# Kernel optimization log

Hardware: AMD Instinct MI355X
Metric: run time of the kernel (lower is better)

Reference implementation:

```python
import jax, jax.numpy as jnp
import numpy as np

B, S, D, H = 4, 2048, 1024, 16
HD = D // H  # head_dim = 64


def setup_inputs() -> dict:
    key = jax.random.key(0)
    ks = jax.random.split(key, 6)
    scale = 0.02
    x = jax.random.normal(ks[0], (B, S, D), dtype=jnp.float32)
    # per-head projection weights, torch Linear is y = x @ W.T; store as [H, D, HD]
    Wq = jax.random.normal(ks[1], (H, D, HD), dtype=jnp.float32) * scale
    Wk = jax.random.normal(ks[2], (H, D, HD), dtype=jnp.float32) * scale
    Wv = jax.random.normal(ks[3], (H, D, HD), dtype=jnp.float32) * scale
    Wo = jax.random.normal(ks[4], (D, D), dtype=jnp.float32) * scale  # torch [out, in]
    bo = jax.random.normal(ks[5], (D,), dtype=jnp.float32) * scale
    return {"x": x, "Wq": Wq, "Wk": Wk, "Wv": Wv, "Wo": Wo, "bo": bo}


def reference(x, Wq, Wk, Wv, Wo, bo):
    # project: [B,S,D] x [H,D,HD] -> [B,H,S,HD]
    q = jnp.einsum("bsd,hde->bhse", x, Wq)
    k = jnp.einsum("bsd,hde->bhse", x, Wk)
    v = jnp.einsum("bsd,hde->bhse", x, Wv)
    scores = jnp.einsum("bhse,bhte->bhst", q, k) / jnp.sqrt(jnp.float32(HD))
    causal = jnp.tril(jnp.ones((S, S), dtype=bool))  # same as registered tril mask
    scores = jnp.where(causal, scores, -jnp.inf)
    w = jax.nn.softmax(scores, axis=-1)
    out = jnp.einsum("bhst,bhte->bhse", w, v)  # [B,H,S,HD]
    # concat heads along feature dim: [B,S,H*HD] = [B,S,D]
    out = out.transpose(0, 2, 1, 3).reshape(B, S, D)
    # output projection: torch Linear y = x @ W.T + b
    return jnp.einsum("bsd,od->bso", out, Wo) + bo
```

## Files before the change

### kernel.cpp

```cpp
#include <hip/hip_runtime.h>
#include <hip/hip_bf16.h>

typedef __bf16 bf16x8 __attribute__((ext_vector_type(8)));
typedef float f32x4 __attribute__((ext_vector_type(4)));
typedef unsigned short u16x4 __attribute__((ext_vector_type(4)));
typedef unsigned short u16x8 __attribute__((ext_vector_type(8)));
typedef unsigned uint4v __attribute__((ext_vector_type(4)));

#define B_ 4
#define S_ 2048
#define D_ 1024
#define H_ 16
#define HD_ 64

__device__ __forceinline__ unsigned short f2bf(float f) {
  unsigned u = __float_as_uint(f);
  u += 0x7fff + ((u >> 16) & 1);
  return (unsigned short)(u >> 16);
}

__device__ __forceinline__ void gload16(const void* g, void* l) {
  __builtin_amdgcn_global_load_lds((const __attribute__((address_space(1))) unsigned int*)g,
                                   (__attribute__((address_space(3))) unsigned int*)l,
                                   16, 0, 0);
}

__global__ void pack_x_k(const float* __restrict__ in, unsigned short* __restrict__ out, int n4) {
  int i = blockIdx.x * blockDim.x + threadIdx.x;
  int stride = gridDim.x * blockDim.x;
  for (; i < n4; i += stride) {
    float4 v = reinterpret_cast<const float4*>(in)[i];
    u16x4 o = {f2bf(v.x), f2bf(v.y), f2bf(v.z), f2bf(v.w)};
    reinterpret_cast<u16x4*>(out)[i] = o;
  }
}

__global__ void pack_wqkv_k(const float* __restrict__ Wq, const float* __restrict__ Wk,
                            const float* __restrict__ Wv, unsigned short* __restrict__ Wt) {
  int o = blockIdx.x * blockDim.x + threadIdx.x;
  int n = o >> 10;
  int d = o & 1023;
  const float* W = (n < 1024) ? Wq : (n < 2048) ? Wk : Wv;
  int nn = n & 1023;
  int h = nn >> 6, e = nn & 63;
  Wt[o] = f2bf(W[(h << 16) + (d << 6) + e]);
}

__global__ __launch_bounds__(512, 2) void gemm256_k(const unsigned short* __restrict__ A,
                                                    const unsigned short* __restrict__ Bt,
                                                    unsigned short* __restrict__ QK,
                                                    unsigned short* __restrict__ VT,
                                                    int M, int N, int K) {
  __shared__ __align__(16) unsigned short lA0[2][128 * 64];
  __shared__ __align__(16) unsigned short lA1[2][128 * 64];
  __shared__ __align__(16) unsigned short lB[2][192 * 64];
  const int tid = threadIdx.x;
  const int wid = tid >> 6, lane = tid & 63;
  const int r = lane & 15, g = lane >> 4;
  const int wm = wid >> 2, wn = wid & 3;

  const int i_hw = blockIdx.y * gridDim.x + blockIdx.x;
  const int xcd = i_hw & 7, j = i_hw >> 3;
  const long arow0 = (long)((xcd & 3) * 8 + (j & 7)) * 256;
  const long bcol0 = (long)((xcd >> 2) * 8 + (j >> 3)) * 192;

  const f32x4 z4 = {0.f, 0.f, 0.f, 0.f};
  f32x4 acc[8][3];
#pragma unroll
  for (int m = 0; m < 8; ++m)
#pragma unroll
    for (int n = 0; n < 3; ++n) acc[m][n] = z4;

  auto stage_half = [&](int kt, int which) {
    const unsigned short* src = (which == 2) ? Bt + bcol0 * K : A + (arow0 + 128 * which) * K;
    const int k0 = kt << 6;
    unsigned short* base = (which == 0) ? &lA0[kt & 1][0]
                         : (which == 1) ? &lA1[kt & 1][0] : &lB[kt & 1][0];
    const int nch = (which == 2) ? 3 : 2;
    for (int c = 0; c < nch; ++c) {
      const int jj = c * 512 + tid;
      const int row = jj >> 3, cc = jj & 7;
      const int ccs = cc ^ (row & 7);
      gload16(src + (long)row * K + k0 + ccs * 8, base + jj * 8);
    }
  };

  bf16x8 af[4][2], bv[3][2];
  auto read_a = [&](const unsigned short* lbase) {
#pragma unroll
    for (int i2 = 0; i2 < 4; ++i2)
#pragma unroll
      for (int kk = 0; kk < 2; ++kk) {
        const int rowh = (2 * i2 + wm) * 16 + r;
        af[i2][kk] = *(const bf16x8*)&lbase[rowh * 64 + (((kk << 2) + g) ^ (rowh & 7)) * 8];
      }
  };
  auto read_b = [&](int buf) {
#pragma unroll
    for (int j2 = 0; j2 < 3; ++j2)
#pragma unroll
      for (int kk = 0; kk < 2; ++kk) {
        const int rowh = (4 * j2 + wn) * 16 + r;
        bv[j2][kk] = *(const bf16x8*)&lB[buf][rowh * 64 + (((kk << 2) + g) ^ (rowh & 7)) * 8];
      }
  };
  auto mma_h = [&](int mh) {
    __builtin_amdgcn_s_setprio(1);
#pragma unroll
    for (int kk = 0; kk < 2; ++kk)
#pragma unroll
      for (int i2 = 0; i2 < 4; ++i2)
#pragma unroll
        for (int j2 = 0; j2 < 3; ++j2)
          acc[4 * mh + i2][j2] = __builtin_amdgcn_mfma_f32_16x16x32_bf16(
              af[i2][kk], bv[j2][kk], acc[4 * mh + i2][j2], 0, 0, 0);
    __builtin_amdgcn_s_setprio(0);
  };

  const int nk = K >> 6;
  stage_half(0, 0);
  stage_half(0, 2);
  stage_half(0, 1);
  asm volatile("s_waitcnt vmcnt(2)" ::: "memory");
  asm volatile("s_barrier" ::: "memory");

  for (int t = 0; t < nk; ++t) {
    const int buf = t & 1;
    const bool pre = (t + 1 < nk);
    read_a(&lA0[buf][0]);
    read_b(buf);
    if (pre) { stage_half(t + 1, 0); stage_half(t + 1, 2); }
    asm volatile("s_barrier" ::: "memory");
    mma_h(0);
    if (pre) asm volatile("s_waitcnt vmcnt(5)" ::: "memory");
    else     asm volatile("s_waitcnt vmcnt(0)" ::: "memory");
    asm volatile("s_waitcnt lgkmcnt(0)\n\ts_barrier" ::: "memory");
    read_a(&lA1[buf][0]);
    if (pre) stage_half(t + 1, 1);
    asm volatile("s_barrier" ::: "memory");
    mma_h(1);
    if (pre) asm volatile("s_waitcnt vmcnt(2)" ::: "memory");
    asm volatile("s_waitcnt lgkmcnt(0)\n\ts_barrier" ::: "memory");
  }

#pragma unroll
  for (int j2 = 0; j2 < 3; ++j2) {
    const long colb = bcol0 + (4 * j2 + wn) * 16;
    if (colb < 2048) {
#pragma unroll
      for (int m = 0; m < 8; ++m)
#pragma unroll
        for (int rr = 0; rr < 4; ++rr) {
          const long row = arow0 + (2 * m + wm) * 16 + g * 4 + rr;
          QK[row * 2048 + colb + r] = f2bf(acc[m][j2][rr]);
        }
    } else {
      const long vcol = colb - 2048 + r;
      const long h = vcol >> 6, e = vcol & 63;
#pragma unroll
      for (int m = 0; m < 8; ++m) {
        const long row0 = arow0 + (2 * m + wm) * 16 + g * 4;
        const long b = row0 >> 11, s = row0 & 2047;
        u16x4 w4;
#pragma unroll
        for (int rr = 0; rr < 4; ++rr) w4[rr] = f2bf(acc[m][j2][rr]);
        *(u16x4*)&VT[(((b << 4) + h) * 64 + e) * 2048 + s] = w4;
      }
    }
  }
}

__global__ __launch_bounds__(512, 2) void gemm_op_k(const unsigned short* __restrict__ A,
                                                    const unsigned short* __restrict__ Bt,
                                                    float* __restrict__ C,
                                                    const float* __restrict__ bias,
                                                    int M, int N, int K) {
  __shared__ __align__(16) unsigned short lA0[2][128 * 64];
  __shared__ __align__(16) unsigned short lA1[2][128 * 64];
  __shared__ __align__(16) unsigned short lB[2][128 * 64];
  const int tid = threadIdx.x;
  const int wid = tid >> 6, lane = tid & 63;
  const int r = lane & 15, g = lane >> 4;
  const int wm = wid >> 2, wn = wid & 3;

  const int i_hw = blockIdx.y * gridDim.x + blockIdx.x;
  const int xcd = i_hw & 7, j = i_hw >> 3;
  const long arow0 = (long)((xcd & 3) * 8 + (j & 7)) * 256;
  const long bcol0 = (long)((xcd >> 2) * 4 + (j >> 3)) * 128;

  const f32x4 z4 = {0.f, 0.f, 0.f, 0.f};
  f32x4 acc[8][2];
#pragma unroll
  for (int m = 0; m < 8; ++m)
#pragma unroll
    for (int n = 0; n < 2; ++n) acc[m][n] = z4;

  auto stage_half = [&](int kt, int which) {
    const unsigned short* src = (which == 2) ? Bt + bcol0 * K : A + (arow0 + 128 * which) * K;
    const int k0 = kt << 6;
    unsigned short* base = (which == 0) ? &lA0[kt & 1][0]
                         : (which == 1) ? &lA1[kt & 1][0] : &lB[kt & 1][0];
#pragma unroll
    for (int c = 0; c < 2; ++c) {
      const int jj = c * 512 + tid;
      const int row = jj >> 3, cc = jj & 7;
      const int ccs = cc ^ (row & 7);
      gload16(src + (long)row * K + k0 + ccs * 8, base + jj * 8);
    }
  };

  bf16x8 af[4][2], bv[2][2];
  auto read_a = [&](const unsigned short* lbase) {
#pragma unroll
    for (int i2 = 0; i2 < 4; ++i2)
#pragma unroll
      for (int kk = 0; kk < 2; ++kk) {
        const int rowh = (2 * i2 + wm) * 16 + r;
        af[i2][kk] = *(const bf16x8*)&lbase[rowh * 64 + (((kk << 2) + g) ^ (rowh & 7)) * 8];
      }
  };
  auto read_b = [&](int buf) {
#pragma unroll
    for (int j2 = 0; j2 < 2; ++j2)
#pragma unroll
      for (int kk = 0; kk < 2; ++kk) {
        const int rowh = (4 * j2 + wn) * 16 + r;
        bv[j2][kk] = *(const bf16x8*)&lB[buf][rowh * 64 + (((kk << 2) + g) ^ (rowh & 7)) * 8];
      }
  };
  auto mma_h = [&](int mh) {
    __builtin_amdgcn_s_setprio(1);
#pragma unroll
    for (int kk = 0; kk < 2; ++kk)
#pragma unroll
      for (int i2 = 0; i2 < 4; ++i2)
#pragma unroll
        for (int j2 = 0; j2 < 2; ++j2)
          acc[4 * mh + i2][j2] = __builtin_amdgcn_mfma_f32_16x16x32_bf16(
              af[i2][kk], bv[j2][kk], acc[4 * mh + i2][j2], 0, 0, 0);
    __builtin_amdgcn_s_setprio(0);
  };

  const int nk = K >> 6;
  stage_half(0, 0);
  stage_half(0, 2);
  stage_half(0, 1);
  asm volatile("s_waitcnt vmcnt(2)" ::: "memory");
  asm volatile("s_barrier" ::: "memory");

  for (int t = 0; t < nk; ++t) {
    const int buf = t & 1;
    const bool pre = (t + 1 < nk);
    read_a(&lA0[buf][0]);
    read_b(buf);
    if (pre) { stage_half(t + 1, 0); stage_half(t + 1, 2); }
    asm volatile("s_barrier" ::: "memory");
    mma_h(0);
    if (pre) asm volatile("s_waitcnt vmcnt(4)" ::: "memory");
    else     asm volatile("s_waitcnt vmcnt(0)" ::: "memory");
    asm volatile("s_waitcnt lgkmcnt(0)\n\ts_barrier" ::: "memory");
    read_a(&lA1[buf][0]);
    if (pre) stage_half(t + 1, 1);
    asm volatile("s_barrier" ::: "memory");
    mma_h(1);
    if (pre) asm volatile("s_waitcnt vmcnt(2)" ::: "memory");
    asm volatile("s_waitcnt lgkmcnt(0)\n\ts_barrier" ::: "memory");
  }

#pragma unroll
  for (int m = 0; m < 8; ++m)
#pragma unroll
    for (int n = 0; n < 2; ++n)
#pragma unroll
      for (int rr = 0; rr < 4; ++rr) {
        const long row = arow0 + (2 * m + wm) * 16 + g * 4 + rr;
        const long col = bcol0 + (4 * n + wn) * 16 + r;
        C[row * N + col] = acc[m][n][rr] + bias[col];
      }
}

__global__ __launch_bounds__(256, 2) void attn_k(const unsigned short* __restrict__ qk,
                                                 const unsigned short* __restrict__ vt,
                                                 unsigned short* __restrict__ out) {
  __shared__ __align__(16) unsigned short lK[2][64 * 64];
  __shared__ __align__(16) unsigned short lVt[2][64 * 64];

  const int tid = threadIdx.x, wid = tid >> 6, lane = tid & 63;
  const int r = lane & 15, g = lane >> 4;
  const int bh = blockIdx.x;
  const int b = bh >> 4, h = bh & 15;
  const int qb = 15 - (int)blockIdx.y;
  const int q0 = qb * 128;

  const unsigned short* Qg = qk + ((long)b * S_) * 2048 + h * 64;
  const unsigned short* Kg = Qg + 1024;
  const unsigned short* Vg = vt + ((long)(b * 16 + h)) * 64 * 2048;

  int qrow[2];
  bf16x8 qf[2][2];
#pragma unroll
  for (int qs = 0; qs < 2; ++qs) {
    qrow[qs] = q0 + qs * 64 + wid * 16 + r;
#pragma unroll
    for (int kk = 0; kk < 2; ++kk)
      qf[qs][kk] = *(const bf16x8*)&Qg[(long)qrow[qs] * 2048 + kk * 32 + g * 8];
  }

  const f32x4 z4 = {0.f, 0.f, 0.f, 0.f};
  f32x4 o[2][4];
#pragma unroll
  for (int qs = 0; qs < 2; ++qs)
#pragma unroll
    for (int nt = 0; nt < 4; ++nt) o[qs][nt] = z4;
  float m_i[2] = {-1e30f, -1e30f};
  float l_i[2] = {0.f, 0.f};

  const int srow = tid >> 3, scc = tid & 7;
  const int sccs = (scc ^ (srow & 7)) << 3;
  const unsigned short* kp = Kg + (long)srow * 2048 + sccs;
  const unsigned short* kp2 = Kg + (long)(srow + 32) * 2048 + sccs;
  const unsigned short* vp = Vg + (long)srow * 2048 + sccs;
  const unsigned short* vp2 = Vg + (long)(srow + 32) * 2048 + sccs;
  auto stage = [&](int buf, long koff, long voff) {
    gload16(kp + koff, &lK[buf][tid * 8]);
    gload16(kp2 + koff, &lK[buf][(256 + tid) * 8]);
    gload16(vp + voff, &lVt[buf][tid * 8]);
    gload16(vp2 + voff, &lVt[buf][(256 + tid) * 8]);
  };

  const int ntiles = (q0 >> 6) + 2;
  stage(0, 0, 0);

  for (int t = 0; t < ntiles; ++t) {
    const int cur = t & 1;
    __syncthreads();
    if (t + 1 < ntiles) stage(cur ^ 1, (long)(t + 1) * 64 * 2048, (long)(t + 1) * 64);

    const int t0 = t << 6;
    const bool act0 = (t < ntiles - 1);
    const bool diag0 = (t == ntiles - 2);
    const bool diag1 = (t == ntiles - 1);

    f32x4 st[2][4];
#pragma unroll
    for (int tt = 0; tt < 4; ++tt) { st[0][tt] = z4; st[1][tt] = z4; }
    __builtin_amdgcn_s_setprio(1);
#pragma unroll
    for (int kk = 0; kk < 2; ++kk)
#pragma unroll
      for (int tt = 0; tt < 4; ++tt) {
        const int row = tt * 16 + r, cc = kk * 4 + g;
        bf16x8 kf = *(const bf16x8*)&lK[cur][(row * 8 + (cc ^ (row & 7))) * 8];
        st[1][tt] = __builtin_amdgcn_mfma_f32_16x16x32_bf16(kf, qf[1][kk], st[1][tt], 0, 0, 0);
        if (act0)
          st[0][tt] = __builtin_amdgcn_mfma_f32_16x16x32_bf16(kf, qf[0][kk], st[0][tt], 0, 0, 0);
      }
    __builtin_amdgcn_s_setprio(0);

    bf16x8 pf[2][2];
    unsigned corr_bits[2] = {0x3f800000u, 0x3f800000u};
    bool dodef[2] = {true, true};
#pragma unroll
    for (int qs = 0; qs < 2; ++qs) {
      if (qs == 0 && !act0) continue;
      const bool diag = qs ? diag1 : diag0;
      float sv[16];
      if (diag) {
#pragma unroll
        for (int tt = 0; tt < 4; ++tt)
#pragma unroll
          for (int rg = 0; rg < 4; ++rg) {
            float s = st[qs][tt][rg];
            if (t0 + tt * 16 + g * 4 + rg > qrow[qs]) s = -1e30f;
            sv[tt * 4 + rg] = s;
          }
      } else {
#pragma unroll
        for (int tt = 0; tt < 4; ++tt)
#pragma unroll
          for (int rg = 0; rg < 4; ++rg) sv[tt * 4 + rg] = st[qs][tt][rg];
      }
      float h0 = fmaxf(fmaxf(fmaxf(sv[0], sv[1]), fmaxf(sv[2], sv[3])),
                       fmaxf(fmaxf(sv[4], sv[5]), fmaxf(sv[6], sv[7])));
      float h1 = fmaxf(fmaxf(fmaxf(sv[8], sv[9]), fmaxf(sv[10], sv[11])),
                       fmaxf(fmaxf(sv[12], sv[13]), fmaxf(sv[14], sv[15])));
      const float pmax = fmaxf(h0, h1);
      const bool defer = __all(pmax - m_i[qs] <= 64.f);
      float corr = 1.f;
      if (!defer) {
        float mx = fmaxf(pmax, m_i[qs]);
        mx = fmaxf(mx, __shfl_xor(mx, 16, 64));
        mx = fmaxf(mx, __shfl_xor(mx, 32, 64));
        corr = __expf((m_i[qs] - mx) * 0.125f);
        m_i[qs] = mx;
      }
      dodef[qs] = defer;
      corr_bits[qs] = __float_as_uint(corr);
      const float m8 = m_i[qs] * 0.125f;
      float p[16];
      float rs = 0.f;
#pragma unroll
      for (int i = 0; i < 16; ++i) {
        p[i] = __expf(__builtin_fmaf(sv[i], 0.125f, -m8));
        rs += p[i];
      }
      rs += __shfl_xor(rs, 16, 64);
      rs += __shfl_xor(rs, 32, 64);
      l_i[qs] = l_i[qs] * corr + rs;
      unsigned cw[4][2];
#pragma unroll
      for (int tt = 0; tt < 4; ++tt)
#pragma unroll
        for (int e = 0; e < 2; ++e)
          asm("v_cvt_pk_bf16_f32 %0, %1, %2"
              : "=v"(cw[tt][e]) : "v"(p[tt * 4 + 2 * e]), "v"(p[tt * 4 + 2 * e + 1]));
#pragma unroll
      for (int kk = 0; kk < 2; ++kk) {
        unsigned x0 = cw[2 * kk][0], y0 = cw[2 * kk + 1][0];
        unsigned x1 = cw[2 * kk][1], y1 = cw[2 * kk + 1][1];
        asm volatile("v_permlane32_swap_b32 %0, %1" : "+v"(x0), "+v"(y0));
        asm volatile("v_permlane16_swap_b32 %0, %1" : "+v"(x0), "+v"(y0));
        asm volatile("v_permlane32_swap_b32 %0, %1" : "+v"(x1), "+v"(y1));
        asm volatile("v_permlane16_swap_b32 %0, %1" : "+v"(x1), "+v"(y1));
        uint4v w = {x0, x1, y0, y1};
        pf[qs][kk] = *(bf16x8*)&w;
      }
    }
#pragma unroll
    for (int qs = 0; qs < 2; ++qs) {
      if (qs == 0 && !act0) continue;
      if (!dodef[qs]) {
        const float corr = __uint_as_float(corr_bits[qs]);
#pragma unroll
        for (int rr = 0; rr < 4; ++rr) {
          const float c = __shfl(corr, g * 4 + rr, 64);
#pragma unroll
          for (int nt = 0; nt < 4; ++nt) o[qs][nt][rr] *= c;
        }
      }
    }

    __builtin_amdgcn_s_setprio(1);
#pragma unroll
    for (int kk = 0; kk < 2; ++kk)
#pragma unroll
      for (int nt = 0; nt < 4; ++nt) {
        const int row = nt * 16 + r, cc = kk * 4 + g;
        const bf16x8 vf = *(const bf16x8*)&lVt[cur][(row * 8 + (cc ^ (row & 7))) * 8];
        o[1][nt] = __builtin_amdgcn_mfma_f32_16x16x32_bf16(pf[1][kk], vf, o[1][nt], 0, 0, 0);
        if (act0)
          o[0][nt] = __builtin_amdgcn_mfma_f32_16x16x32_bf16(pf[0][kk], vf, o[0][nt], 0, 0, 0);
      }
    __builtin_amdgcn_s_setprio(0);
  }

#pragma unroll
  for (int qs = 0; qs < 2; ++qs) {
    float linv[4];
#pragma unroll
    for (int rr = 0; rr < 4; ++rr)
      linv[rr] = 1.f / __shfl(l_i[qs], g * 4 + rr, 64);
#pragma unroll
    for (int nt = 0; nt < 4; ++nt)
#pragma unroll
      for (int rr = 0; rr < 4; ++rr) {
        const long s = q0 + qs * 64 + wid * 16 + g * 4 + rr;
        out[((long)b * S_ + s) * 1024 + h * 64 + nt * 16 + r] = f2bf(o[qs][nt][rr] * linv[rr]);
      }
  }
}

extern "C" void kernel_launch(void* const* d_in, const int* in_sizes, int n_in,
                              void* d_out, int out_size, void* d_ws, size_t ws_size,
                              hipStream_t stream) {
  const float* x = (const float*)d_in[0];
  const float* Wq = (const float*)d_in[1];
  const float* Wk = (const float*)d_in[2];
  const float* Wv = (const float*)d_in[3];
  const float* Wo = (const float*)d_in[4];
  const float* bo = (const float*)d_in[5];
  float* out = (float*)d_out;

  char* ws = (char*)d_ws;
  unsigned short* Xb = (unsigned short*)(ws);
  unsigned short* Wt = (unsigned short*)(ws + (16ul << 20));
  unsigned short* Wob = (unsigned short*)(ws + (22ul << 20));
  unsigned short* QK = (unsigned short*)(ws + (24ul << 20));
  unsigned short* VT = (unsigned short*)(ws + (56ul << 20));
  unsigned short* AO = (unsigned short*)(ws + (72ul << 20));

  pack_x_k<<<2048, 256, 0, stream>>>(x, Xb, (B_ * S_ * D_) / 4);
  pack_x_k<<<512, 256, 0, stream>>>(Wo, Wob, (D_ * D_) / 4);
  pack_wqkv_k<<<(3 * D_ * D_) / 256, 256, 0, stream>>>(Wq, Wk, Wv, Wt);

  gemm256_k<<<dim3(32, 16), 512, 0, stream>>>(Xb, Wt, QK, VT, B_ * S_, 3 * D_, D_);
  attn_k<<<dim3(64, 16), 256, 0, stream>>>(QK, VT, AO);
  gemm_op_k<<<dim3(32, 8), 512, 0, stream>>>(AO, Wob, out, bo, B_ * S_, D_, D_);
}
```

Before: 178.0 us.

## Shrink attention query tile from 128 to 64 rows per block

```diff
diff --git a/kernel.cpp b/kernel.cpp
--- a/kernel.cpp
+++ b/kernel.cpp
@@ -289,31 +289,25 @@
   const int r = lane & 15, g = lane >> 4;
   const int bh = blockIdx.x;
   const int b = bh >> 4, h = bh & 15;
-  const int qb = 15 - (int)blockIdx.y;
-  const int q0 = qb * 128;
+  const int qb = 31 - (int)blockIdx.y;
+  const int q0 = qb * 64;
 
   const unsigned short* Qg = qk + ((long)b * S_) * 2048 + h * 64;
   const unsigned short* Kg = Qg + 1024;
   const unsigned short* Vg = vt + ((long)(b * 16 + h)) * 64 * 2048;
 
-  int qrow[2];
-  bf16x8 qf[2][2];
-#pragma unroll
-  for (int qs = 0; qs < 2; ++qs) {
-    qrow[qs] = q0 + qs * 64 + wid * 16 + r;
-#pragma unroll
-    for (int kk = 0; kk < 2; ++kk)
-      qf[qs][kk] = *(const bf16x8*)&Qg[(long)qrow[qs] * 2048 + kk * 32 + g * 8];
-  }
+  const int qrow = q0 + wid * 16 + r;
+  bf16x8 qf[2];
+#pragma unroll
+  for (int kk = 0; kk < 2; ++kk)
+    qf[kk] = *(const bf16x8*)&Qg[(long)qrow * 2048 + kk * 32 + g * 8];
 
   const f32x4 z4 = {0.f, 0.f, 0.f, 0.f};
-  f32x4 o[2][4];
-#pragma unroll
-  for (int qs = 0; qs < 2; ++qs)
-#pragma unroll
-    for (int nt = 0; nt < 4; ++nt) o[qs][nt] = z4;
-  float m_i[2] = {-1e30f, -1e30f};
-  float l_i[2] = {0.f, 0.f};
+  f32x4 o[4];
+#pragma unroll
+  for (int nt = 0; nt < 4; ++nt) o[nt] = z4;
+  float m_i = -1e30f;
+  float l_i = 0.f;
 
   const int srow = tid >> 3, scc = tid & 7;
   const int sccs = (scc ^ (srow & 7)) << 3;
@@ -328,7 +322,7 @@
     gload16(vp2 + voff, &lVt[buf][(256 + tid) * 8]);
   };
 
-  const int ntiles = (q0 >> 6) + 2;
+  const int ntiles = qb + 1;
   stage(0, 0, 0);
 
   for (int t = 0; t < ntiles; ++t) {
@@ -337,13 +331,11 @@
     if (t + 1 < ntiles) stage(cur ^ 1, (long)(t + 1) * 64 * 2048, (long)(t + 1) * 64);
 
     const int t0 = t << 6;
-    const bool act0 = (t < ntiles - 1);
-    const bool diag0 = (t == ntiles - 2);
-    const bool diag1 = (t == ntiles - 1);
-
-    f32x4 st[2][4];
-#pragma unroll
-    for (int tt = 0; tt < 4; ++tt) { st[0][tt] = z4; st[1][tt] = z4; }
+    const bool diag = (t == ntiles - 1);
+
+    f32x4 st[4];
+#pragma unroll
+    for (int tt = 0; tt < 4; ++tt) st[tt] = z4;
     __builtin_amdgcn_s_setprio(1);
 #pragma unroll
     for (int kk = 0; kk < 2; ++kk)
@@ -351,92 +343,76 @@
       for (int tt = 0; tt < 4; ++tt) {
         const int row = tt * 16 + r, cc = kk * 4 + g;
         bf16x8 kf = *(const bf16x8*)&lK[cur][(row * 8 + (cc ^ (row & 7))) * 8];
-        st[1][tt] = __builtin_amdgcn_mfma_f32_16x16x32_bf16(kf, qf[1][kk], st[1][tt], 0, 0, 0);
-        if (act0)
-          st[0][tt] = __builtin_amdgcn_mfma_f32_16x16x32_bf16(kf, qf[0][kk], st[0][tt], 0, 0, 0);
+        st[tt] = __builtin_amdgcn_mfma_f32_16x16x32_bf16(kf, qf[kk], st[tt], 0, 0, 0);
       }
     __builtin_amdgcn_s_setprio(0);
 
-    bf16x8 pf[2][2];
-    unsigned corr_bits[2] = {0x3f800000u, 0x3f800000u};
-    bool dodef[2] = {true, true};
-#pragma unroll
-    for (int qs = 0; qs < 2; ++qs) {
-      if (qs == 0 && !act0) continue;
-      const bool diag = qs ? diag1 : diag0;
-      float sv[16];
-      if (diag) {
-#pragma unroll
-        for (int tt = 0; tt < 4; ++tt)
-#pragma unroll
-          for (int rg = 0; rg < 4; ++rg) {
-            float s = st[qs][tt][rg];
-            if (t0 + tt * 16 + g * 4 + rg > qrow[qs]) s = -1e30f;
-            sv[tt * 4 + rg] = s;
-          }
-      } else {
-#pragma unroll
-        for (int tt = 0; tt < 4; ++tt)
-#pragma unroll
-          for (int rg = 0; rg < 4; ++rg) sv[tt * 4 + rg] = st[qs][tt][rg];
-      }
-      float h0 = fmaxf(fmaxf(fmaxf(sv[0], sv[1]), fmaxf(sv[2], sv[3])),
-                       fmaxf(fmaxf(sv[4], sv[5]), fmaxf(sv[6], sv[7])));
-      float h1 = fmaxf(fmaxf(fmaxf(sv[8], sv[9]), fmaxf(sv[10], sv[11])),
-                       fmaxf(fmaxf(sv[12], sv[13]), fmaxf(sv[14], sv[15])));
-      const float pmax = fmaxf(h0, h1);
-      const bool defer = __all(pmax - m_i[qs] <= 64.f);
-      float corr = 1.f;
-      if (!defer) {
-        float mx = fmaxf(pmax, m_i[qs]);
-        mx = fmaxf(mx, __shfl_xor(mx, 16, 64));
-        mx = fmaxf(mx, __shfl_xor(mx, 32, 64));
-        corr = __expf((m_i[qs] - mx) * 0.125f);
-        m_i[qs] = mx;
-      }
-      dodef[qs] = defer;
-      corr_bits[qs] = __float_as_uint(corr);
-      const float m8 = m_i[qs] * 0.125f;
-      float p[16];
-      float rs = 0.f;
-#pragma unroll
-      for (int i = 0; i < 16; ++i) {
-        p[i] = __expf(__builtin_fmaf(sv[i], 0.125f, -m8));
-        rs += p[i];
-      }
-      rs += __shfl_xor(rs, 16, 64);
-      rs += __shfl_xor(rs, 32, 64);
-      l_i[qs] = l_i[qs] * corr + rs;
-      unsigned cw[4][2];
+    float sv[16];
+    if (diag) {
 #pragma unroll
       for (int tt = 0; tt < 4; ++tt)
 #pragma unroll
-        for (int e = 0; e < 2; ++e)
-          asm("v_cvt_pk_bf16_f32 %0, %1, %2"
-              : "=v"(cw[tt][e]) : "v"(p[tt * 4 + 2 * e]), "v"(p[tt * 4 + 2 * e + 1]));
-#pragma unroll
-      for (int kk = 0; kk < 2; ++kk) {
-        unsigned x0 = cw[2 * kk][0], y0 = cw[2 * kk + 1][0];
-        unsigned x1 = cw[2 * kk][1], y1 = cw[2 * kk + 1][1];
-        asm volatile("v_permlane32_swap_b32 %0, %1" : "+v"(x0), "+v"(y0));
-        asm volatile("v_permlane16_swap_b32 %0, %1" : "+v"(x0), "+v"(y0));
-        asm volatile("v_permlane32_swap_b32 %0, %1" : "+v"(x1), "+v"(y1));
-        asm volatile("v_permlane16_swap_b32 %0, %1" : "+v"(x1), "+v"(y1));
-        uint4v w = {x0, x1, y0, y1};
-        pf[qs][kk] = *(bf16x8*)&w;
-      }
-    }
-#pragma unroll
-    for (int qs = 0; qs < 2; ++qs) {
-      if (qs == 0 && !act0) continue;
-      if (!dodef[qs]) {
-        const float corr = __uint_as_float(corr_bits[qs]);
-#pragma unroll
-        for (int rr = 0; rr < 4; ++rr) {
-          const float c = __shfl(corr, g * 4 + rr, 64);
-#pragma unroll
-          for (int nt = 0; nt < 4; ++nt) o[qs][nt][rr] *= c;
+        for (int rg = 0; rg < 4; ++rg) {
+          float s = st[tt][rg];
+          if (t0 + tt * 16 + g * 4 + rg > qrow) s = -1e30f;
+          sv[tt * 4 + rg] = s;
         }
+    } else {
+#pragma unroll
+      for (int tt = 0; tt < 4; ++tt)
+#pragma unroll
+        for (int rg = 0; rg < 4; ++rg) sv[tt * 4 + rg] = st[tt][rg];
+    }
+    float h0 = fmaxf(fmaxf(fmaxf(sv[0], sv[1]), fmaxf(sv[2], sv[3])),
+                     fmaxf(fmaxf(sv[4], sv[5]), fmaxf(sv[6], sv[7])));
+    float h1 = fmaxf(fmaxf(fmaxf(sv[8], sv[9]), fmaxf(sv[10], sv[11])),
+                     fmaxf(fmaxf(sv[12], sv[13]), fmaxf(sv[14], sv[15])));
+    const float pmax = fmaxf(h0, h1);
+    const bool defer = __all(pmax - m_i <= 64.f);
+    float corr = 1.f;
+    if (!defer) {
+      float mx = fmaxf(pmax, m_i);
+      mx = fmaxf(mx, __shfl_xor(mx, 16, 64));
+      mx = fmaxf(mx, __shfl_xor(mx, 32, 64));
+      corr = __expf((m_i - mx) * 0.125f);
+      m_i = mx;
+    }
+    const float m8 = m_i * 0.125f;
+    float p[16];
+    float rs = 0.f;
+#pragma unroll
+    for (int i = 0; i < 16; ++i) {
+      p[i] = __expf(__builtin_fmaf(sv[i], 0.125f, -m8));
+      rs += p[i];
+    }
+    rs += __shfl_xor(rs, 16, 64);
+    rs += __shfl_xor(rs, 32, 64);
+    l_i = l_i * corr + rs;
+    unsigned cw[4][2];
+#pragma unroll
+    for (int tt = 0; tt < 4; ++tt)
+#pragma unroll
+      for (int e = 0; e < 2; ++e)
+        asm("v_cvt_pk_bf16_f32 %0, %1, %2"
+            : "=v"(cw[tt][e]) : "v"(p[tt * 4 + 2 * e]), "v"(p[tt * 4 + 2 * e + 1]));
+    bf16x8 pf[2];
+#pragma unroll
+    for (int kk = 0; kk < 2; ++kk) {
+      unsigned x0 = cw[2 * kk][0], y0 = cw[2 * kk + 1][0];
+      unsigned x1 = cw[2 * kk][1], y1 = cw[2 * kk + 1][1];
+      asm volatile("v_permlane32_swap_b32 %0, %1" : "+v"(x0), "+v"(y0));
+      asm volatile("v_permlane16_swap_b32 %0, %1" : "+v"(x0), "+v"(y0));
+      asm volatile("v_permlane32_swap_b32 %0, %1" : "+v"(x1), "+v"(y1));
+      asm volatile("v_permlane16_swap_b32 %0, %1" : "+v"(x1), "+v"(y1));
+      uint4v w = {x0, x1, y0, y1};
+      pf[kk] = *(bf16x8*)&w;
+    }
+    if (!defer) {
+#pragma unroll
+      for (int rr = 0; rr < 4; ++rr) {
+        const float c = __shfl(corr, g * 4 + rr, 64);
+#pragma unroll
+        for (int nt = 0; nt < 4; ++nt) o[nt][rr] *= c;
       }
     }
 
@@ -447,27 +423,22 @@
       for (int nt = 0; nt < 4; ++nt) {
         const int row = nt * 16 + r, cc = kk * 4 + g;
         const bf16x8 vf = *(const bf16x8*)&lVt[cur][(row * 8 + (cc ^ (row & 7))) * 8];
-        o[1][nt] = __builtin_amdgcn_mfma_f32_16x16x32_bf16(pf[1][kk], vf, o[1][nt], 0, 0, 0);
-        if (act0)
-          o[0][nt] = __builtin_amdgcn_mfma_f32_16x16x32_bf16(pf[0][kk], vf, o[0][nt], 0, 0, 0);
+        o[nt] = __builtin_amdgcn_mfma_f32_16x16x32_bf16(pf[kk], vf, o[nt], 0, 0, 0);
       }
     __builtin_amdgcn_s_setprio(0);
   }
 
-#pragma unroll
-  for (int qs = 0; qs < 2; ++qs) {
-    float linv[4];
-#pragma unroll
-    for (int rr = 0; rr < 4; ++rr)
-      linv[rr] = 1.f / __shfl(l_i[qs], g * 4 + rr, 64);
-#pragma unroll
-    for (int nt = 0; nt < 4; ++nt)
-#pragma unroll
-      for (int rr = 0; rr < 4; ++rr) {
-        const long s = q0 + qs * 64 + wid * 16 + g * 4 + rr;
-        out[((long)b * S_ + s) * 1024 + h * 64 + nt * 16 + r] = f2bf(o[qs][nt][rr] * linv[rr]);
-      }
-  }
+  float linv[4];
+#pragma unroll
+  for (int rr = 0; rr < 4; ++rr)
+    linv[rr] = 1.f / __shfl(l_i, g * 4 + rr, 64);
+#pragma unroll
+  for (int nt = 0; nt < 4; ++nt)
+#pragma unroll
+    for (int rr = 0; rr < 4; ++rr) {
+      const long s = q0 + wid * 16 + g * 4 + rr;
+      out[((long)b * S_ + s) * 1024 + h * 64 + nt * 16 + r] = f2bf(o[nt][rr] * linv[rr]);
+    }
 }
 
 extern "C" void kernel_launch(void* const* d_in, const int* in_sizes, int n_in,
@@ -494,6 +465,6 @@
   pack_wqkv_k<<<(3 * D_ * D_) / 256, 256, 0, stream>>>(Wq, Wk, Wv, Wt);
 
   gemm256_k<<<dim3(32, 16), 512, 0, stream>>>(Xb, Wt, QK, VT, B_ * S_, 3 * D_, D_);
-  attn_k<<<dim3(64, 16), 256, 0, stream>>>(QK, VT, AO);
+  attn_k<<<dim3(64, 32), 256, 0, stream>>>(QK, VT, AO);
   gemm_op_k<<<dim3(32, 8), 512, 0, stream>>>(AO, Wob, out, bo, B_ * S_, D_, D_);
 }
```

After: 175.2 us, median of 2. No clear change (-1.6%).
